# Kernel tuning notes

Hardware: AMD Instinct MI355X
Metric: run time of the kernel (lower is better)

The kernel has to match this reference:

```python
import jax, jax.numpy as jnp
import numpy as np
from jax import lax

GO = 1  # mead-baseline Offsets.GO
NEG = -10000.0


def setup_inputs() -> dict:
    key = jax.random.key(0)
    k1, k2, k3, k4 = jax.random.split(key, 4)
    B, T, K = 1024, 512, 64
    unary = jax.random.normal(k1, (B, T, K), dtype=jnp.float32)
    lengths = jax.random.randint(k2, (B,), 1, T + 1).astype(jnp.int32)
    inv_mask = jax.random.randint(k3, (K, K), 0, 2).astype(jnp.int32)
    A = (jax.random.normal(k4, (K, K), dtype=jnp.float32) * 0.1)
    return {"unary": unary, "lengths": lengths, "inv_mask": inv_mask, "A": A}


def _viterbi(probv, trans, seq_lens):
    """Masked Viterbi decode (tf.contrib.crf.crf_decode semantics).

    probv: [B, T1, K] unary scores (GO frame already prepended)
    trans: [K, K] transition scores, trans[i, j] = score(i -> j)
    seq_lens: [B] int32, valid lengths (already +1 for the GO frame)
    """
    B, T1, K = probv.shape
    alpha0 = probv[:, 0]                      # [B, K]
    us = jnp.swapaxes(probv[:, 1:], 0, 1)     # [T1-1, B, K]
    ts = jnp.arange(1, T1)

    def fwd(alpha, xs):
        u_t, t = xs
        scores = alpha[:, :, None] + trans[None]        # [B, K_prev, K_cur]
        bp = jnp.argmax(scores, axis=1).astype(jnp.int32)  # [B, K]
        new_alpha = jnp.max(scores, axis=1) + u_t
        alpha = jnp.where((t < seq_lens)[:, None], new_alpha, alpha)  # freeze past length
        return alpha, bp

    alpha_f, bps = lax.scan(fwd, alpha0, (us, ts))  # bps: [T1-1, B, K]
    last = jnp.argmax(alpha_f, axis=-1).astype(jnp.int32)  # [B] tag at last valid step
    best = jnp.max(alpha_f, axis=-1)                       # [B]

    def bwd(tag, xs):
        bp_t, t = xs
        prev = jnp.take_along_axis(bp_t, tag[:, None], axis=1)[:, 0]
        prev = jnp.where(t < seq_lens, prev, tag)  # beyond length: carry tag back
        return prev, prev

    _, prevs = lax.scan(bwd, last, (bps[::-1], ts[::-1]))  # prevs: [T1-1, B] (times T1-2..0)
    tags = jnp.concatenate([prevs[::-1], last[None]], axis=0)  # [T1, B]
    return jnp.swapaxes(tags, 0, 1), best


def reference(unary, lengths, inv_mask, A):
    B, T, K = unary.shape
    inv = inv_mask.astype(jnp.float32) * NEG
    trans = jax.nn.log_softmax(A + inv, axis=-1)
    gos = jnp.full((1, 1, K), NEG, dtype=unary.dtype).at[:, :, GO].set(0.0)
    probv = jnp.concatenate([jnp.broadcast_to(gos, (B, 1, K)), unary], axis=1)  # [B, T+1, K]
    viterbi, _ = _viterbi(probv, trans, lengths.astype(jnp.int32) + 1)
    return viterbi[:, 1:]  # drop GO position -> [B, T]
```

## Files before the change

### kernel.cpp

```cpp
#include <hip/hip_runtime.h>

#define NEGV -10000.0f
#define BB 1024
#define TT 512
#define KK 64

typedef float vf2 __attribute__((ext_vector_type(2)));

#define BAR() asm volatile("s_waitcnt lgkmcnt(0)\n\ts_barrier" ::: "memory")

__global__ __launch_bounds__(64)
void trans_kernel(const float* __restrict__ A, const int* __restrict__ inv,
                  float* __restrict__ trans)
{
    const int i = blockIdx.x, j = threadIdx.x;
    float x = A[i * KK + j] + (inv[i * KK + j] ? NEGV : 0.0f);
    float m = x;
    #pragma unroll
    for (int o = 32; o > 0; o >>= 1) m = fmaxf(m, __shfl_xor(m, o));
    float e = expf(x - m);
    float s = e;
    #pragma unroll
    for (int o = 32; o > 0; o >>= 1) s += __shfl_xor(s, o);
    trans[i * KK + j] = (x - m) - logf(s);
}


__device__ __forceinline__ int imin3(int a, int b, int c) { return min(min(a, b), c); }

#define FILL4(BUF_, RB_)                                                       \
  { _Pragma("unroll")                                                          \
    for (int d_ = 0; d_ < 4; ++d_) {                                           \
        int r_ = (RB_) + d_; if (r_ > TT - 1) r_ = TT - 1;                     \
        BUF_[d_] = ur[r_ * KK + j];                                            \
    } }

#define STEP(T_, UV_)                                                          \
  {                                                                            \
                      \
    float sv[32];                                                              \
    _Pragma("unroll")                                                          \
    for (int q = 0; q < 8; ++q) {                                              \
        vf2 t01 = vf2{a4[q].x, a4[q].y} + Tr2[2 * q];                          \
        vf2 t23 = vf2{a4[q].z, a4[q].w} + Tr2[2 * q + 1];                      \
        sv[4 * q + 0] = t01.x; sv[4 * q + 1] = t01.y;                          \
        sv[4 * q + 2] = t23.x; sv[4 * q + 3] = t23.y;                          \
    }                                                                          \
                                          \
    float l0[11];                                                              \
    _Pragma("unroll")                                                          \
    for (int i = 0; i < 10; ++i)                                               \
        l0[i] = fmaxf(fmaxf(sv[3 * i], sv[3 * i + 1]), sv[3 * i + 2]);         \
    l0[10] = fmaxf(sv[30], sv[31]);                                            \
    float l1a = fmaxf(fmaxf(l0[0], l0[1]), l0[2]);                             \
    float l1b = fmaxf(fmaxf(l0[3], l0[4]), l0[5]);                             \
    float l1c = fmaxf(fmaxf(l0[6], l0[7]), l0[8]);                             \
    float l1d = fmaxf(l0[9], l0[10]);                                          \
    float mw  = fmaxf(fmaxf(fmaxf(l1a, l1b), l1c), l1d);                       \
       \
    int c[32];                                                                 \
    _Pragma("unroll")                                                          \
    for (int i = 0; i < 32; ++i) c[i] = (sv[i] == mw) ? i : 32;                \
    int n0[11];                                                                \
    _Pragma("unroll")                                                          \
    for (int i = 0; i < 10; ++i)                                               \
        n0[i] = imin3(c[3 * i], c[3 * i + 1], c[3 * i + 2]);                   \
    n0[10] = min(c[30], c[31]);                                                \
    int n1a = imin3(n0[0], n0[1], n0[2]);                                      \
    int n1b = imin3(n0[3], n0[4], n0[5]);                                      \
    int n1c = imin3(n0[6], n0[7], n0[8]);                                      \
    int n1d = min(n0[9], n0[10]);                                              \
    int gidx = min(min(min(n1a, n1b), n1c), n1d) + ibase;                      \
     \
    float mo = __shfl_xor(mw, 32);                                             \
    int   go = __shfl_xor(gidx, 32);                                           \
    bool take = ishi ? (mo >= mw) : (mo > mw);                                 \
    float m  = fmaxf(mw, mo);                                                  \
    int  bpi = take ? go : gidx;                                               \
    float u_ = (UV_);                                                          \
    asm volatile("" : "+v"(u_));                                               \
    if ((T_) <= len) alpha = m + u_;         \
    if (!ishi) sA[j] = alpha;                  \
    else if ((T_) >= 2 && (T_) <= len)                                         \
        sbp[((T_) - 2) * KK + j] = (unsigned char)bpi;       \
    BAR();             \
    {                                                                          \
        const float4* p = (const float4*)sA + (ibase >> 2);                    \
        _Pragma("unroll")                                                      \
        for (int q = 0; q < 8; ++q) a4[q] = p[q];                              \
    }                                                                          \
  }

__global__ __launch_bounds__(128, 2)
void viterbi_kernel(const float* __restrict__ unary, const int* __restrict__ lengths,
                    const float* __restrict__ trans, int* __restrict__ out)
{
    const int tid   = threadIdx.x;
    const int wv    = tid >> 6;
    const int lane  = tid & 63;
    const int sub   = lane & 31;
    const int ibase = (lane >> 5) << 5;
    const bool ishi = (lane >= 32);
    const int j     = wv * 32 + sub;
    const int b     = blockIdx.x;

    __shared__ unsigned char sbp[(TT - 1) * KK];
    __shared__ __align__(16) float sA[KK];

    vf2 Tr2[16];
    #pragma unroll
    for (int q = 0; q < 16; ++q) {
        Tr2[q].x = trans[(ibase + 2 * q)     * KK + j];
        Tr2[q].y = trans[(ibase + 2 * q + 1) * KK + j];
    }

    const int len = lengths[b];
    const float* ur = unary + (long)b * (TT * KK);
    int* orow = out + b * TT;

    float ub0[4], ub1[4];
    FILL4(ub0, 0) FILL4(ub1, 4)

    float alpha = (j == 1) ? 0.0f : NEGV;
    if (!ishi) sA[j] = alpha;
    BAR();

    float4 a4[8];
    {
        const float4* p = (const float4*)sA + (ibase >> 2);
        #pragma unroll
        for (int q = 0; q < 8; ++q) a4[q] = p[q];
    }

    for (int tb = 1; tb <= len; tb += 8) {
        STEP(tb + 0, ub0[0]) STEP(tb + 1, ub0[1])
        STEP(tb + 2, ub0[2]) STEP(tb + 3, ub0[3])
        FILL4(ub0, tb + 7)
        STEP(tb + 4, ub1[0]) STEP(tb + 5, ub1[1])
        STEP(tb + 6, ub1[2]) STEP(tb + 7, ub1[3])
        FILL4(ub1, tb + 11)
    }

    if (wv == 1) return;

    float av = sA[lane];
    float mm = av;
    #pragma unroll
    for (int o = 32; o > 0; o >>= 1) mm = fmaxf(mm, __shfl_xor(mm, o));
    unsigned long long msk = __ballot(av == mm);
    int last = __ffsll(msk) - 1;

    for (int jj = len - 1 + lane; jj < TT; jj += 64) orow[jj] = last;

    asm volatile("s_waitcnt lgkmcnt(0)" ::: "memory");

    int tag = last;
    for (int t = len; t >= 2; --t) {
        int prev = sbp[(t - 2) * KK + tag];
        if (lane == 0) orow[t - 2] = prev;
        tag = prev;
    }
}

extern "C" void kernel_launch(void* const* d_in, const int* in_sizes, int n_in,
                              void* d_out, int out_size, void* d_ws, size_t ws_size,
                              hipStream_t stream)
{
    const float* unary   = (const float*)d_in[0];
    const int*   lengths = (const int*)d_in[1];
    const int*   inv     = (const int*)d_in[2];
    const float* A       = (const float*)d_in[3];
    int*         out     = (int*)d_out;

    float* trans = (float*)d_ws;

    trans_kernel<<<KK, KK, 0, stream>>>(A, inv, trans);
    viterbi_kernel<<<BB, 128, 0, stream>>>(unary, lengths, trans, out);
}
```

Before: 440.9 us.

## Run Viterbi recurrence in a single wave per sequence, dropping barriers

Each batch row now runs in one 64-lane wavefront instead of two waves that split the previous-state range. Each lane keeps all 64 transition values for its column and reduces over all 64 predecessors itself, using packed two-wide max trees. This removes the cross-lane shuffle merge and replaces the block barrier with a plain LDS wait. The argmax search is moved after the next alpha vector is read, so it is off the critical dependency chain. In exchange each lane does twice the ALU work per step and holds more registers, and the launch bounds drop to one wave per block.

New measurement: 523.7 us. 1.19x slower.

```diff
diff --git a/kernel.cpp b/kernel.cpp
--- a/kernel.cpp
+++ b/kernel.cpp
@@ -7,7 +7,11 @@
 
 typedef float vf2 __attribute__((ext_vector_type(2)));
 
-#define BAR() asm volatile("s_waitcnt lgkmcnt(0)\n\ts_barrier" ::: "memory")
+__device__ __forceinline__ vf2 vmax2(vf2 a, vf2 b)
+{
+    return vf2{fmaxf(a.x, b.x), fmaxf(a.y, b.y)};
+}
+__device__ __forceinline__ int imin3(int a, int b, int c) { return min(min(a, b), c); }
 
 __global__ __launch_bounds__(64)
 void trans_kernel(const float* __restrict__ A, const int* __restrict__ inv,
@@ -26,8 +30,6 @@
 }
 
 
-__device__ __forceinline__ int imin3(int a, int b, int c) { return min(min(a, b), c); }
-
 #define FILL4(BUF_, RB_)                                                       \
   { _Pragma("unroll")                                                          \
     for (int d_ = 0; d_ < 4; ++d_) {                                           \
@@ -37,81 +39,77 @@
 
 #define STEP(T_, UV_)                                                          \
   {                                                                            \
-                      \
-    float sv[32];                                                              \
+      \
+    vf2 sv2[32];                                                               \
     _Pragma("unroll")                                                          \
-    for (int q = 0; q < 8; ++q) {                                              \
-        vf2 t01 = vf2{a4[q].x, a4[q].y} + Tr2[2 * q];                          \
-        vf2 t23 = vf2{a4[q].z, a4[q].w} + Tr2[2 * q + 1];                      \
-        sv[4 * q + 0] = t01.x; sv[4 * q + 1] = t01.y;                          \
-        sv[4 * q + 2] = t23.x; sv[4 * q + 3] = t23.y;                          \
+    for (int q = 0; q < 16; ++q) {                                             \
+        sv2[2 * q]     = vf2{av[q].x, av[q].y} + Tr2[2 * q];                   \
+        sv2[2 * q + 1] = vf2{av[q].z, av[q].w} + Tr2[2 * q + 1];               \
     }                                                                          \
-                                          \
-    float l0[11];                                                              \
+                     \
+    vf2 x16[16];                                                               \
     _Pragma("unroll")                                                          \
-    for (int i = 0; i < 10; ++i)                                               \
-        l0[i] = fmaxf(fmaxf(sv[3 * i], sv[3 * i + 1]), sv[3 * i + 2]);         \
-    l0[10] = fmaxf(sv[30], sv[31]);                                            \
-    float l1a = fmaxf(fmaxf(l0[0], l0[1]), l0[2]);                             \
-    float l1b = fmaxf(fmaxf(l0[3], l0[4]), l0[5]);                             \
-    float l1c = fmaxf(fmaxf(l0[6], l0[7]), l0[8]);                             \
-    float l1d = fmaxf(l0[9], l0[10]);                                          \
-    float mw  = fmaxf(fmaxf(fmaxf(l1a, l1b), l1c), l1d);                       \
-       \
-    int c[32];                                                                 \
+    for (int i = 0; i < 16; ++i) x16[i] = vmax2(sv2[i], sv2[i + 16]);          \
+    vf2 x8[8];                                                                 \
     _Pragma("unroll")                                                          \
-    for (int i = 0; i < 32; ++i) c[i] = (sv[i] == mw) ? i : 32;                \
-    int n0[11];                                                                \
+    for (int i = 0; i < 8; ++i) x8[i] = vmax2(x16[i], x16[i + 8]);             \
+    vf2 x4[4];                                                                 \
     _Pragma("unroll")                                                          \
-    for (int i = 0; i < 10; ++i)                                               \
-        n0[i] = imin3(c[3 * i], c[3 * i + 1], c[3 * i + 2]);                   \
-    n0[10] = min(c[30], c[31]);                                                \
-    int n1a = imin3(n0[0], n0[1], n0[2]);                                      \
-    int n1b = imin3(n0[3], n0[4], n0[5]);                                      \
-    int n1c = imin3(n0[6], n0[7], n0[8]);                                      \
-    int n1d = min(n0[9], n0[10]);                                              \
-    int gidx = min(min(min(n1a, n1b), n1c), n1d) + ibase;                      \
-     \
-    float mo = __shfl_xor(mw, 32);                                             \
-    int   go = __shfl_xor(gidx, 32);                                           \
-    bool take = ishi ? (mo >= mw) : (mo > mw);                                 \
-    float m  = fmaxf(mw, mo);                                                  \
-    int  bpi = take ? go : gidx;                                               \
+    for (int i = 0; i < 4; ++i) x4[i] = vmax2(x8[i], x8[i + 4]);               \
+    vf2 x2a = vmax2(x4[0], x4[2]), x2b = vmax2(x4[1], x4[3]);                  \
+    vf2 x1  = vmax2(x2a, x2b);                                                 \
+    const float m = fmaxf(x1.x, x1.y);                  \
     float u_ = (UV_);                                                          \
     asm volatile("" : "+v"(u_));                                               \
     if ((T_) <= len) alpha = m + u_;         \
-    if (!ishi) sA[j] = alpha;                  \
-    else if ((T_) >= 2 && (T_) <= len)                                         \
-        sbp[((T_) - 2) * KK + j] = (unsigned char)bpi;       \
-    BAR();             \
+    sA[j] = alpha;                                                             \
+       \
+       \
+    asm volatile("s_waitcnt lgkmcnt(0)" ::: "memory");                         \
     {                                                                          \
-        const float4* p = (const float4*)sA + (ibase >> 2);                    \
+        const float4* p = (const float4*)sA;                                   \
         _Pragma("unroll")                                                      \
-        for (int q = 0; q < 8; ++q) a4[q] = p[q];                              \
+        for (int q = 0; q < 16; ++q) av[q] = p[q];                             \
+    }                                                                          \
+           \
+    {                                                                          \
+        int c[64];                                                             \
+        _Pragma("unroll")                                                      \
+        for (int i = 0; i < 64; ++i)                                           \
+            c[i] = (sv2[i >> 1][i & 1] == m) ? i : 64;                         \
+        int m0[22];                                                            \
+        _Pragma("unroll")                                                      \
+        for (int i = 0; i < 21; ++i)                                           \
+            m0[i] = imin3(c[3 * i], c[3 * i + 1], c[3 * i + 2]);               \
+        m0[21] = c[63];                                                        \
+        int m1[8];                                                             \
+        _Pragma("unroll")                                                      \
+        for (int i = 0; i < 7; ++i)                                            \
+            m1[i] = imin3(m0[3 * i], m0[3 * i + 1], m0[3 * i + 2]);            \
+        m1[7] = m0[21];                                                        \
+        int bpi = imin3(imin3(m1[0], m1[1], m1[2]),                            \
+                        imin3(m1[3], m1[4], m1[5]),                            \
+                        min(m1[6], m1[7]));                                    \
+        if ((T_) >= 2 && (T_) <= len)                                          \
+            sbp[((T_) - 2) * KK + j] = (unsigned char)bpi;                     \
     }                                                                          \
   }
 
-__global__ __launch_bounds__(128, 2)
+__global__ __launch_bounds__(64, 1)
 void viterbi_kernel(const float* __restrict__ unary, const int* __restrict__ lengths,
                     const float* __restrict__ trans, int* __restrict__ out)
 {
-    const int tid   = threadIdx.x;
-    const int wv    = tid >> 6;
-    const int lane  = tid & 63;
-    const int sub   = lane & 31;
-    const int ibase = (lane >> 5) << 5;
-    const bool ishi = (lane >= 32);
-    const int j     = wv * 32 + sub;
-    const int b     = blockIdx.x;
+    const int j = threadIdx.x;
+    const int b = blockIdx.x;
 
     __shared__ unsigned char sbp[(TT - 1) * KK];
     __shared__ __align__(16) float sA[KK];
 
-    vf2 Tr2[16];
+    vf2 Tr2[32];
     #pragma unroll
-    for (int q = 0; q < 16; ++q) {
-        Tr2[q].x = trans[(ibase + 2 * q)     * KK + j];
-        Tr2[q].y = trans[(ibase + 2 * q + 1) * KK + j];
+    for (int p = 0; p < 32; ++p) {
+        Tr2[p].x = trans[(2 * p)     * KK + j];
+        Tr2[p].y = trans[(2 * p + 1) * KK + j];
     }
 
     const int len = lengths[b];
@@ -122,14 +120,14 @@
     FILL4(ub0, 0) FILL4(ub1, 4)
 
     float alpha = (j == 1) ? 0.0f : NEGV;
-    if (!ishi) sA[j] = alpha;
-    BAR();
+    sA[j] = alpha;
+    asm volatile("s_waitcnt lgkmcnt(0)" ::: "memory");
 
-    float4 a4[8];
+    float4 av[16];
     {
-        const float4* p = (const float4*)sA + (ibase >> 2);
+        const float4* p = (const float4*)sA;
         #pragma unroll
-        for (int q = 0; q < 8; ++q) a4[q] = p[q];
+        for (int q = 0; q < 16; ++q) av[q] = p[q];
     }
 
     for (int tb = 1; tb <= len; tb += 8) {
@@ -141,23 +139,20 @@
         FILL4(ub1, tb + 11)
     }
 
-    if (wv == 1) return;
-
-    float av = sA[lane];
-    float mm = av;
+    float mm = alpha;
     #pragma unroll
     for (int o = 32; o > 0; o >>= 1) mm = fmaxf(mm, __shfl_xor(mm, o));
-    unsigned long long msk = __ballot(av == mm);
+    unsigned long long msk = __ballot(alpha == mm);
     int last = __ffsll(msk) - 1;
 
-    for (int jj = len - 1 + lane; jj < TT; jj += 64) orow[jj] = last;
+    for (int jj = len - 1 + j; jj < TT; jj += 64) orow[jj] = last;
 
     asm volatile("s_waitcnt lgkmcnt(0)" ::: "memory");
 
     int tag = last;
     for (int t = len; t >= 2; --t) {
         int prev = sbp[(t - 2) * KK + tag];
-        if (lane == 0) orow[t - 2] = prev;
+        if (j == 0) orow[t - 2] = prev;
         tag = prev;
     }
 }
@@ -175,5 +170,5 @@
     float* trans = (float*)d_ws;
 
     trans_kernel<<<KK, KK, 0, stream>>>(A, inv, trans);
-    viterbi_kernel<<<BB, 128, 0, stream>>>(unary, lengths, trans, out);
+    viterbi_kernel<<<BB, 64, 0, stream>>>(unary, lengths, trans, out);
 }
```
